# Performance work log

Measured on AMD Instinct MI355X. Metric: run time of the kernel, lower is better.

The kernel has to match this reference:

```python
import jax, jax.numpy as jnp
import numpy as np

B, S, H, NH, HD, V = 2, 2048, 1024, 16, 64, 32000
BASE = 10000.0
NEG = jnp.finfo(jnp.float32).min


def setup_inputs() -> dict:
    key = jax.random.key(0)
    ks = jax.random.split(key, 12)
    batch = jax.random.randint(ks[0], (B, S), 0, V)
    positions = jnp.broadcast_to(jnp.arange(S), (B, S))
    lengths = jax.random.randint(ks[1], (B,), 1, S + 1)  # >=1 to avoid fully-masked rows
    sc = 1.0 / np.sqrt(H)
    emb = jax.random.normal(ks[2], (V, H), dtype=jnp.float32) * 0.02
    wq = jax.random.normal(ks[3], (H, NH * HD), dtype=jnp.float32) * sc
    bq = jnp.zeros((NH * HD,), jnp.float32)
    wk = jax.random.normal(ks[4], (H, NH * HD), dtype=jnp.float32) * sc
    bk = jnp.zeros((NH * HD,), jnp.float32)
    wv = jax.random.normal(ks[5], (H, NH * HD), dtype=jnp.float32) * sc
    bv = jnp.zeros((NH * HD,), jnp.float32)
    wo = jax.random.normal(ks[6], (NH * HD, H), dtype=jnp.float32) * sc
    bo = jnp.zeros((H,), jnp.float32)
    return dict(batch=batch, positions=positions, lengths=lengths, emb=emb,
                wq=wq, bq=bq, wk=wk, bk=bk, wv=wv, bv=bv, wo=wo, bo=bo)


def _rope(x, positions):
    # x: [B, NH, S, HD]; positions: [B, S] int
    inv_freq = 1.0 / (BASE ** (jnp.arange(0, HD, 2, dtype=jnp.float32) / HD))  # [HD/2]
    freqs = positions.astype(jnp.float32)[..., None] * inv_freq               # [B, S, HD/2]
    ang = jnp.concatenate([freqs, freqs], axis=-1)                            # [B, S, HD]
    cos = jnp.cos(ang)[:, None]                                               # [B, 1, S, HD]
    sin = jnp.sin(ang)[:, None]
    x1, x2 = x[..., :HD // 2], x[..., HD // 2:]
    rot = jnp.concatenate([-x2, x1], axis=-1)
    return x * cos + rot * sin


def reference(batch, positions, lengths, emb, wq, bq, wk, bk, wv, bv, wo, bo):
    h = emb[batch]                                                 # [B, S, H]
    q = (h @ wq + bq).reshape(B, S, NH, HD).transpose(0, 2, 1, 3)  # [B, NH, S, HD]
    k = (h @ wk + bk).reshape(B, S, NH, HD).transpose(0, 2, 1, 3)
    v = (h @ wv + bv).reshape(B, S, NH, HD).transpose(0, 2, 1, 3)
    q = _rope(q, positions)
    k = _rope(k, positions)
    scores = jnp.einsum('bhqd,bhkd->bhqk', q, k) / np.sqrt(HD)     # [B, NH, S, S]
    causal = jnp.triu(jnp.full((S, S), NEG, jnp.float32), 1)
    pad = jnp.where(jnp.arange(S)[None, :] < lengths[:, None], 0.0, NEG)  # [B, S]
    mask = pad[:, None, None, :] + causal[None, None]              # [B, 1, S, S]
    attn = jax.nn.softmax(scores + mask, axis=-1)
    out = jnp.einsum('bhqk,bhkd->bhqd', attn, v)                   # [B, NH, S, HD]
    out = out.transpose(0, 2, 1, 3).reshape(B, S, NH * HD)
    return out @ wo + bo                                           # [B, S, H]
```

## Files before the change

### kernel.cpp

```cpp
#include <hip/hip_runtime.h>
#include <hip/hip_bf16.h>
#include <cstdint>

#define DEVINL __device__ __forceinline__

typedef __attribute__((ext_vector_type(8))) short short8;
typedef __attribute__((ext_vector_type(4))) short bhalf4;
typedef __attribute__((ext_vector_type(4))) float f32x4;

constexpr int B_ = 2, S_ = 2048, H_ = 1024, NH_ = 16, HD_ = 64;
constexpr int M_ = B_ * S_;
constexpr float SCALE = 0.125f;

DEVINL float bf2f(unsigned short h) {
    unsigned u = ((unsigned)h) << 16;
    float f; __builtin_memcpy(&f, &u, 4); return f;
}
DEVINL unsigned short f2bf(float f) {
    unsigned u; __builtin_memcpy(&u, &f, 4);
    u += 0x7FFFu + ((u >> 16) & 1u);
    return (unsigned short)(u >> 16);
}
DEVINL float ldin(const void* p, size_t i, int fp32) {
    return fp32 ? ((const float*)p)[i] : bf2f(((const unsigned short*)p)[i]);
}
DEVINL void gl16(const void* g, void* l) {
    __builtin_amdgcn_global_load_lds(
        (const __attribute__((address_space(1))) unsigned int*)g,
        (__attribute__((address_space(3))) unsigned int*)l, 16, 0, 0);
}
DEVINL f32x4 mfma16(short8 a, short8 b, f32x4 c) {
    return __builtin_amdgcn_mfma_f32_16x16x32_bf16(a, b, c, 0, 0, 0);
}
DEVINL f32x4 mfma16x16(bhalf4 a, bhalf4 b, f32x4 c) {
#if __has_builtin(__builtin_amdgcn_mfma_f32_16x16x16bf16_1k)
    return __builtin_amdgcn_mfma_f32_16x16x16bf16_1k(a, b, c, 0, 0, 0);
#else
    f32x4 d;
    asm volatile("v_mfma_f32_16x16x16_bf16 %0, %1, %2, %3\n\t"
                 "s_nop 7\n\ts_nop 7"
                 : "=v"(d) : "v"(a), "v"(b), "v"(c));
    return d;
#endif
}
DEVINL void fsincos(float rev01, float* sn, float* cs) {
#if __has_builtin(__builtin_amdgcn_sinf) && __has_builtin(__builtin_amdgcn_cosf)
    *sn = __builtin_amdgcn_sinf(rev01);
    *cs = __builtin_amdgcn_cosf(rev01);
#else
    float a = rev01 * 6.28318530717958647692f;
    *sn = __sinf(a); *cs = __cosf(a);
#endif
}

__global__ __launch_bounds__(256) void k_detect(const unsigned short* __restrict__ emb,
                                                int* __restrict__ flag) {
    int t = threadIdx.x;
    unsigned short hw = emb[2 * t];
    unsigned e = (hw >> 7) & 0xFFu;
    int plaus = ((e >= 90u) && (e <= 126u)) || ((hw & 0x7FFFu) == 0u);
    __shared__ int cnt[4];
    int s = plaus;
    #pragma unroll
    for (int o = 1; o < 64; o <<= 1) s += __shfl_xor(s, o);
    if ((t & 63) == 0) cnt[t >> 6] = s;
    __syncthreads();
    if (t == 0) flag[0] = ((cnt[0] + cnt[1] + cnt[2] + cnt[3]) > 192) ? 0 : 1;
}

__global__ __launch_bounds__(256) void k_bias(const void* bq, const void* bk,
                                              const void* bv, const void* bo,
                                              const int* __restrict__ flag,
                                              float* __restrict__ out) {
    int i = blockIdx.x * 256 + threadIdx.x;
    int fp32 = flag[0];
    const void* src = (i < 1024) ? bq : (i < 2048) ? bk : (i < 3072) ? bv : bo;
    out[i] = ldin(src, (size_t)(i & 1023), fp32);
}

__global__ __launch_bounds__(256) void k_transw(const void* w0, const void* w1,
                                                const void* w2, const void* w3,
                                                const int* __restrict__ flag,
                                                unsigned short* __restrict__ wT) {
    __shared__ float tile[32][33];
    int mat = blockIdx.z;
    const void* w = (mat == 0) ? w0 : (mat == 1) ? w1 : (mat == 2) ? w2 : w3;
    int fp32 = flag[0];
    int n0 = blockIdx.x * 32, k0 = blockIdx.y * 32;
    int tx = threadIdx.x, ty = threadIdx.y;
    for (int i = ty; i < 32; i += 8)
        tile[i][tx] = ldin(w, (size_t)(k0 + i) * 1024 + n0 + tx, fp32);
    __syncthreads();
    unsigned short* dst = wT + (size_t)mat * 1024 * 1024;
    for (int i = ty; i < 32; i += 8)
        dst[(size_t)(n0 + i) * 1024 + k0 + tx] = f2bf(tile[tx][i]);
}

__global__ __launch_bounds__(256) void k_gather(const int* __restrict__ batch,
                                                const void* __restrict__ emb,
                                                const int* __restrict__ flag,
                                                unsigned short* __restrict__ h) {
    int row = blockIdx.x, t = threadIdx.x;
    int tok = batch[row];
    unsigned short* dst = h + (size_t)row * H_;
    if (flag[0]) {
        const float4* s = (const float4*)((const float*)emb + (size_t)tok * H_);
        float4 x = s[t];
        unsigned long long pk = (unsigned long long)f2bf(x.x)
                              | ((unsigned long long)f2bf(x.y) << 16)
                              | ((unsigned long long)f2bf(x.z) << 32)
                              | ((unsigned long long)f2bf(x.w) << 48);
        ((unsigned long long*)dst)[t] = pk;
    } else {
        ((uint2*)dst)[t] =
            ((const uint2*)((const unsigned short*)emb + (size_t)tok * H_))[t];
    }
}

__global__ __launch_bounds__(256) void k_gemm_qkv(const unsigned short* __restrict__ A,
                                                  const unsigned short* __restrict__ Bt,
                                                  const float* __restrict__ bias,
                                                  const int* __restrict__ positions,
                                                  unsigned short* __restrict__ qo,
                                                  unsigned short* __restrict__ ko,
                                                  unsigned short* __restrict__ vo) {
    constexpr int K = 1024;
    __shared__ alignas(16) unsigned short As[128 * 32];
    __shared__ alignas(16) unsigned short Bs[128 * 32];
    int t = threadIdx.x, lane = t & 63, quad = lane >> 4, n16 = lane & 15;
    int w = t >> 6, wm = w >> 1, wn = w & 1;
    int m0 = blockIdx.y * 128, n0 = blockIdx.x * 128;
    f32x4 acc[4][4];
    #pragma unroll
    for (int mi = 0; mi < 4; mi++)
        #pragma unroll
        for (int ni = 0; ni < 4; ni++) acc[mi][ni] = (f32x4){0.f, 0.f, 0.f, 0.f};
    int c0 = t, c1 = t + 256;
    int ra0 = c0 >> 2, ka0 = (c0 & 3) * 8;
    int ra1 = c1 >> 2, ka1 = (c1 & 3) * 8;
    for (int k0 = 0; k0 < K; k0 += 32) {
        __syncthreads();
        gl16(A  + (size_t)(m0 + ra0) * K + k0 + ka0, &As[c0 * 8]);
        gl16(A  + (size_t)(m0 + ra1) * K + k0 + ka1, &As[c1 * 8]);
        gl16(Bt + (size_t)(n0 + ra0) * K + k0 + ka0, &Bs[c0 * 8]);
        gl16(Bt + (size_t)(n0 + ra1) * K + k0 + ka1, &Bs[c1 * 8]);
        __syncthreads();
        short8 af[4], bfr[4];
        #pragma unroll
        for (int mi = 0; mi < 4; mi++)
            af[mi] = *(const short8*)&As[(wm * 64 + mi * 16 + n16) * 32 + quad * 8];
        #pragma unroll
        for (int ni = 0; ni < 4; ni++)
            bfr[ni] = *(const short8*)&Bs[(wn * 64 + ni * 16 + n16) * 32 + quad * 8];
        #pragma unroll
        for (int mi = 0; mi < 4; mi++)
            #pragma unroll
            for (int ni = 0; ni < 4; ni++)
                acc[mi][ni] = mfma16(af[mi], bfr[ni], acc[mi][ni]);
    }
    int colbase = n0 + wn * 64;
    int buf = colbase >> 10;
    unsigned short* out = (buf == 0) ? qo : (buf == 1) ? ko : vo;
    int cc = colbase & 1023;
    float bb[4];
    #pragma unroll
    for (int ni = 0; ni < 4; ni++) bb[ni] = bias[colbase + ni * 16 + n16];
    if (buf == 2) {
        #pragma unroll
        for (int mi = 0; mi < 4; mi++)
            #pragma unroll
            for (int ni = 0; ni < 4; ni++) {
                int row = m0 + wm * 64 + mi * 16 + quad * 4;
                #pragma unroll
                for (int i = 0; i < 4; i++)
                    out[(size_t)(row + i) * 1024 + cc + ni * 16 + n16] =
                        f2bf(acc[mi][ni][i] + bb[ni]);
            }
    } else {
        float revf[2];
        #pragma unroll
        for (int ni = 0; ni < 2; ni++) {
            float d = (float)(ni * 16 + n16);
            revf[ni] = __expf(d * -0.28782313f) * 0.15915494f;
        }
        #pragma unroll
        for (int mi = 0; mi < 4; mi++) {
            int row0 = m0 + wm * 64 + mi * 16 + quad * 4;
            #pragma unroll
            for (int i = 0; i < 4; i++) {
                int row = row0 + i;
                float pos = (float)positions[row];
                #pragma unroll
                for (int ni = 0; ni < 2; ni++) {
                    float rev = pos * revf[ni];
                    float fr = rev - floorf(rev);
                    float sn, cs; fsincos(fr, &sn, &cs);
                    float x1 = acc[mi][ni][i] + bb[ni];
                    float x2 = acc[mi][ni + 2][i] + bb[ni + 2];
                    out[(size_t)row * 1024 + cc + ni * 16 + n16] = f2bf(x1 * cs - x2 * sn);
                    out[(size_t)row * 1024 + cc + (ni + 2) * 16 + n16] = f2bf(x2 * cs + x1 * sn);
                }
            }
        }
    }
}

__global__ __launch_bounds__(256) void k_attn(const unsigned short* __restrict__ q,
                                              const unsigned short* __restrict__ k_,
                                              const unsigned short* __restrict__ v,
                                              const int* __restrict__ lengths,
                                              unsigned short* __restrict__ o) {
    __shared__ alignas(16) unsigned short Ks[64 * 64];
    __shared__ alignas(16) unsigned short Vt[64 * 68];
    int bx = blockIdx.x;
    int j = bx & 15, hh = (bx >> 4) & 15, b = bx >> 8;
    int t = threadIdx.x, w = t >> 6, lane = t & 63, quad = lane >> 4, n16 = lane & 15;
    int len = lengths[b];
    int tile0 = j, tile1 = 31 - j;
    int kend0 = min(tile0 * 64 + 64, len);
    int kend1 = min(tile1 * 64 + 64, len);
    int nkt = (kend1 + 63) >> 6;
    int qrow0 = tile0 * 64 + w * 16 + n16;
    int qrow1 = tile1 * 64 + w * 16 + n16;
    int limit0 = min(qrow0, len - 1);
    int limit1 = min(qrow1, len - 1);
    short8 qf[2][2];
    {
        size_t qa = ((size_t)(b * S_ + qrow0)) * H_ + hh * 64 + quad * 8;
        size_t qb2 = ((size_t)(b * S_ + qrow1)) * H_ + hh * 64 + quad * 8;
        qf[0][0] = *(const short8*)(q + qa);  qf[0][1] = *(const short8*)(q + qa + 32);
        qf[1][0] = *(const short8*)(q + qb2); qf[1][1] = *(const short8*)(q + qb2 + 32);
    }
    f32x4 oa[2][4];
    float m_[2], l_[2];
    #pragma unroll
    for (int s = 0; s < 2; s++) {
        m_[s] = -__builtin_inff(); l_[s] = 0.f;
        #pragma unroll
        for (int nb = 0; nb < 4; nb++) oa[s][nb] = (f32x4){0.f, 0.f, 0.f, 0.f};
    }
    int vkey = t >> 3, vc = t & 7;
    for (int kt = 0; kt < nkt; kt++) {
        int kb = kt * 64;
        __syncthreads();
        {
            int s0 = t;        int ky = s0 >> 3; int ch = (s0 & 7) ^ (ky & 7);
            gl16(k_ + ((size_t)(b * S_ + kb + ky)) * H_ + hh * 64 + ch * 8, &Ks[s0 * 8]);
            int s1 = t + 256;  ky = s1 >> 3;     ch = (s1 & 7) ^ (ky & 7);
            gl16(k_ + ((size_t)(b * S_ + kb + ky)) * H_ + hh * 64 + ch * 8, &Ks[s1 * 8]);
        }
        #pragma unroll
        for (int hlf = 0; hlf < 2; hlf++) {
            int ky = vkey + hlf * 32;
            short8 vv = *(const short8*)(v + ((size_t)(b * S_ + kb + ky)) * H_ + hh * 64 + vc * 8);
            int slot = ky ^ ((vc >> 1) << 2);
            #pragma unroll
            for (int jj = 0; jj < 8; jj++)
                Vt[(vc * 8 + jj) * 68 + slot] = (unsigned short)vv[jj];
        }
        __syncthreads();
        short8 kf[4][2];
        #pragma unroll
        for (int st = 0; st < 4; st++)
            #pragma unroll
            for (int hf = 0; hf < 2; hf++) {
                int ky = st * 16 + n16;
                int slot = ky * 8 + ((hf * 4 + quad) ^ (ky & 7));
                kf[st][hf] = *(const short8*)&Ks[slot * 8];
            }
        bhalf4 vf[4][4];
        #pragma unroll
        for (int st = 0; st < 4; st++)
            #pragma unroll
            for (int nb = 0; nb < 4; nb++) {
                int slot = (st * 16 + quad * 4) ^ (nb << 2);
                vf[st][nb] = *(const bhalf4*)&Vt[(nb * 16 + n16) * 68 + slot];
            }
        #pragma unroll
        for (int si = 0; si < 2; si++) {
            if (si == 0 && kb >= kend0) continue;
            int limit = si ? limit1 : limit0;
            f32x4 sc[4];
            #pragma unroll
            for (int st = 0; st < 4; st++) {
                f32x4 z = (f32x4){0.f, 0.f, 0.f, 0.f};
                z = mfma16(kf[st][0], qf[si][0], z);
                z = mfma16(kf[st][1], qf[si][1], z);
                sc[st] = z;
            }
            float mx = -__builtin_inff();
            #pragma unroll
            for (int st = 0; st < 4; st++)
                #pragma unroll
                for (int i = 0; i < 4; i++) {
                    int kg = kb + st * 16 + quad * 4 + i;
                    float val = sc[st][i] * SCALE;
                    val = (kg <= limit) ? val : -__builtin_inff();
                    sc[st][i] = val;
                    mx = fmaxf(mx, val);
                }
            mx = fmaxf(mx, __shfl_xor(mx, 16));
            mx = fmaxf(mx, __shfl_xor(mx, 32));
            float mnew = fmaxf(m_[si], mx);
            float alpha = __expf(m_[si] - mnew);
            m_[si] = mnew;
            float rs = 0.f;
            bhalf4 pf[4];
            #pragma unroll
            for (int st = 0; st < 4; st++)
                #pragma unroll
                for (int i = 0; i < 4; i++) {
                    float p = __expf(sc[st][i] - mnew);
                    rs += p;
                    pf[st][i] = (short)f2bf(p);
                }
            rs += __shfl_xor(rs, 16);
            rs += __shfl_xor(rs, 32);
            l_[si] = alpha * l_[si] + rs;
            f32x4 av;
            #pragma unroll
            for (int i = 0; i < 4; i++) av[i] = __shfl(alpha, quad * 4 + i);
            #pragma unroll
            for (int nb = 0; nb < 4; nb++) oa[si][nb] *= av;
            #pragma unroll
            for (int st = 0; st < 4; st++)
                #pragma unroll
                for (int nb = 0; nb < 4; nb++)
                    oa[si][nb] = mfma16x16(pf[st], vf[st][nb], oa[si][nb]);
        }
    }
    #pragma unroll
    for (int si = 0; si < 2; si++) {
        int tb = si ? tile1 : tile0;
        f32x4 rl;
        #pragma unroll
        for (int i = 0; i < 4; i++) rl[i] = 1.f / __shfl(l_[si], quad * 4 + i);
        #pragma unroll
        for (int nb = 0; nb < 4; nb++) {
            #pragma unroll
            for (int i = 0; i < 4; i++) {
                int row = tb * 64 + w * 16 + quad * 4 + i;
                o[((size_t)(b * S_ + row)) * H_ + hh * 64 + nb * 16 + n16] =
                    f2bf(oa[si][nb][i] * rl[i]);
            }
        }
    }
}

__global__ __launch_bounds__(256) void k_gemm64(const unsigned short* __restrict__ A,
                                                const unsigned short* __restrict__ Bt,
                                                const float* __restrict__ bias,
                                                unsigned short* __restrict__ Cb,
                                                float* __restrict__ Cf,
                                                const int* __restrict__ flag) {
    constexpr int K = 1024, N = 1024;
    __shared__ alignas(16) unsigned short As[64 * 32];
    __shared__ alignas(16) unsigned short Bs[128 * 32];
    int t = threadIdx.x, lane = t & 63, quad = lane >> 4, n16 = lane & 15;
    int w = t >> 6, wm = w & 1, wn = w >> 1;
    int m0 = blockIdx.y * 64, n0 = blockIdx.x * 128;
    f32x4 acc[2][4];
    #pragma unroll
    for (int mi = 0; mi < 2; mi++)
        #pragma unroll
        for (int ni = 0; ni < 4; ni++) acc[mi][ni] = (f32x4){0.f, 0.f, 0.f, 0.f};
    int ra = t >> 2, ka = (t & 3) * 8;
    int rb1 = (t + 256) >> 2, kb1 = ((t + 256) & 3) * 8;
    for (int k0 = 0; k0 < K; k0 += 32) {
        __syncthreads();
        gl16(A  + (size_t)(m0 + ra) * K + k0 + ka, &As[t * 8]);
        gl16(Bt + (size_t)(n0 + ra) * K + k0 + ka, &Bs[t * 8]);
        gl16(Bt + (size_t)(n0 + rb1) * K + k0 + kb1, &Bs[(t + 256) * 8]);
        __syncthreads();
        short8 af[2], bfr[4];
        #pragma unroll
        for (int mi = 0; mi < 2; mi++)
            af[mi] = *(const short8*)&As[(wm * 32 + mi * 16 + n16) * 32 + quad * 8];
        #pragma unroll
        for (int ni = 0; ni < 4; ni++)
            bfr[ni] = *(const short8*)&Bs[(wn * 64 + ni * 16 + n16) * 32 + quad * 8];
        #pragma unroll
        for (int mi = 0; mi < 2; mi++)
            #pragma unroll
            for (int ni = 0; ni < 4; ni++)
                acc[mi][ni] = mfma16(af[mi], bfr[ni], acc[mi][ni]);
    }
    int fp32out = (flag[0] == 1);
    #pragma unroll
    for (int mi = 0; mi < 2; mi++) {
        #pragma unroll
        for (int ni = 0; ni < 4; ni++) {
            int row = m0 + wm * 32 + mi * 16 + quad * 4;
            int col = n0 + wn * 64 + ni * 16 + n16;
            float bb = bias[col];
            #pragma unroll
            for (int i = 0; i < 4; i++) {
                float val = acc[mi][ni][i] + bb;
                size_t idx = (size_t)(row + i) * N + col;
                if (fp32out) Cf[idx] = val;
                else         Cb[idx] = f2bf(val);
            }
        }
    }
}

extern "C" void kernel_launch(void* const* d_in, const int* in_sizes, int n_in,
                              void* d_out, int out_size, void* d_ws, size_t ws_size,
                              hipStream_t stream) {
    (void)in_sizes; (void)n_in; (void)out_size; (void)ws_size;
    const int* batch     = (const int*)d_in[0];
    const int* positions = (const int*)d_in[1];
    const int* lengths   = (const int*)d_in[2];
    const void* emb = d_in[3];
    const void* wq = d_in[4];  const void* bq = d_in[5];
    const void* wk = d_in[6];  const void* bk = d_in[7];
    const void* wv = d_in[8];  const void* bv = d_in[9];
    const void* wo = d_in[10]; const void* bo = d_in[11];

    char* ws = (char*)d_ws;
    int*   flag   = (int*)ws;
    float* biasws = (float*)(ws + 4096);
    unsigned short* wT = (unsigned short*)(ws + 20480);
    size_t off = 20480 + (8ull << 20);
    unsigned short* hbuf = (unsigned short*)(ws + off); off += (8ull << 20);
    unsigned short* qb   = (unsigned short*)(ws + off); off += (8ull << 20);
    unsigned short* kb2  = (unsigned short*)(ws + off); off += (8ull << 20);
    unsigned short* vb   = (unsigned short*)(ws + off); off += (8ull << 20);
    unsigned short* ao   = (unsigned short*)(ws + off); off += (8ull << 20);

    k_detect<<<1, 256, 0, stream>>>((const unsigned short*)emb, flag);
    k_bias<<<16, 256, 0, stream>>>(bq, bk, bv, bo, flag, biasws);
    k_transw<<<dim3(32, 32, 4), dim3(32, 8), 0, stream>>>(wq, wk, wv, wo, flag, wT);
    k_gather<<<M_, 256, 0, stream>>>(batch, emb, flag, hbuf);

    k_gemm_qkv<<<dim3(3072 / 128, M_ / 128), 256, 0, stream>>>(
        hbuf, wT, biasws, positions, qb, kb2, vb);

    k_attn<<<B_ * NH_ * 16, 256, 0, stream>>>(qb, kb2, vb, lengths, ao);

    k_gemm64<<<dim3(1024 / 128, M_ / 64), 256, 0, stream>>>(
        ao, wT + (3ull << 20), biasws + 3072,
        (unsigned short*)d_out, (float*)d_out, flag);
}
```

Baseline: 323.1 us.

## Write V transposed from QKV GEMM, fuse detect into bias, deepen K-step

The QKV GEMM epilogue now writes V transposed ([B, feature, seq]), so attention can load V tiles with direct global-to-LDS copies instead of a register transpose. The P·V product switches from the 16x16x16 MFMA to the 16x16x32 MFMA. Both GEMMs now load 64-wide K chunks per barrier pair, halving the number of synchronizations. The dtype-detect kernel is merged into the bias kernel, and for bf16 inputs the gather is skipped by indexing the embedding rows directly in the GEMM. The trade-offs are more LDS use per block and an epilogue V store with a large stride.

```diff
diff --git a/kernel.cpp b/kernel.cpp
--- a/kernel.cpp
+++ b/kernel.cpp
@@ -31,17 +31,6 @@
 }
 DEVINL f32x4 mfma16(short8 a, short8 b, f32x4 c) {
     return __builtin_amdgcn_mfma_f32_16x16x32_bf16(a, b, c, 0, 0, 0);
-}
-DEVINL f32x4 mfma16x16(bhalf4 a, bhalf4 b, f32x4 c) {
-#if __has_builtin(__builtin_amdgcn_mfma_f32_16x16x16bf16_1k)
-    return __builtin_amdgcn_mfma_f32_16x16x16bf16_1k(a, b, c, 0, 0, 0);
-#else
-    f32x4 d;
-    asm volatile("v_mfma_f32_16x16x16_bf16 %0, %1, %2, %3\n\t"
-                 "s_nop 7\n\ts_nop 7"
-                 : "=v"(d) : "v"(a), "v"(b), "v"(c));
-    return d;
-#endif
 }
 DEVINL void fsincos(float rev01, float* sn, float* cs) {
 #if __has_builtin(__builtin_amdgcn_sinf) && __has_builtin(__builtin_amdgcn_cosf)
@@ -52,28 +41,27 @@
     *sn = __sinf(a); *cs = __cosf(a);
 #endif
 }
-
-__global__ __launch_bounds__(256) void k_detect(const unsigned short* __restrict__ emb,
-                                                int* __restrict__ flag) {
-    int t = threadIdx.x;
+DEVINL int detect_fp32(const unsigned short* emb, int t) {
     unsigned short hw = emb[2 * t];
     unsigned e = (hw >> 7) & 0xFFu;
-    int plaus = ((e >= 90u) && (e <= 126u)) || ((hw & 0x7FFFu) == 0u);
+    int s = (((e >= 90u) && (e <= 126u)) || ((hw & 0x7FFFu) == 0u)) ? 1 : 0;
+    #pragma unroll
+    for (int o = 1; o < 64; o <<= 1) s += __shfl_xor(s, o);
     __shared__ int cnt[4];
-    int s = plaus;
-    #pragma unroll
-    for (int o = 1; o < 64; o <<= 1) s += __shfl_xor(s, o);
     if ((t & 63) == 0) cnt[t >> 6] = s;
     __syncthreads();
-    if (t == 0) flag[0] = ((cnt[0] + cnt[1] + cnt[2] + cnt[3]) > 192) ? 0 : 1;
+    return ((cnt[0] + cnt[1] + cnt[2] + cnt[3]) > 192) ? 0 : 1;
 }
 
 __global__ __launch_bounds__(256) void k_bias(const void* bq, const void* bk,
                                               const void* bv, const void* bo,
-                                              const int* __restrict__ flag,
+                                              const unsigned short* __restrict__ emb,
+                                              int* __restrict__ flag,
                                               float* __restrict__ out) {
-    int i = blockIdx.x * 256 + threadIdx.x;
-    int fp32 = flag[0];
+    int t = threadIdx.x;
+    int fp32 = detect_fp32(emb, t);
+    if (blockIdx.x == 0 && t == 0) flag[0] = fp32;
+    int i = blockIdx.x * 256 + t;
     const void* src = (i < 1024) ? bq : (i < 2048) ? bk : (i < 3072) ? bv : bo;
     out[i] = ldin(src, (size_t)(i & 1023), fp32);
 }
@@ -100,83 +88,103 @@
                                                 const void* __restrict__ emb,
                                                 const int* __restrict__ flag,
                                                 unsigned short* __restrict__ h) {
+    if (flag[0] == 0) return;
     int row = blockIdx.x, t = threadIdx.x;
     int tok = batch[row];
-    unsigned short* dst = h + (size_t)row * H_;
-    if (flag[0]) {
-        const float4* s = (const float4*)((const float*)emb + (size_t)tok * H_);
-        float4 x = s[t];
-        unsigned long long pk = (unsigned long long)f2bf(x.x)
-                              | ((unsigned long long)f2bf(x.y) << 16)
-                              | ((unsigned long long)f2bf(x.z) << 32)
-                              | ((unsigned long long)f2bf(x.w) << 48);
-        ((unsigned long long*)dst)[t] = pk;
-    } else {
-        ((uint2*)dst)[t] =
-            ((const uint2*)((const unsigned short*)emb + (size_t)tok * H_))[t];
-    }
-}
-
-__global__ __launch_bounds__(256) void k_gemm_qkv(const unsigned short* __restrict__ A,
+    const float4* s = (const float4*)((const float*)emb + (size_t)tok * H_);
+    float4 x = s[t];
+    unsigned long long pk = (unsigned long long)f2bf(x.x)
+                          | ((unsigned long long)f2bf(x.y) << 16)
+                          | ((unsigned long long)f2bf(x.z) << 32)
+                          | ((unsigned long long)f2bf(x.w) << 48);
+    ((unsigned long long*)(h + (size_t)row * H_))[t] = pk;
+}
+
+__global__ __launch_bounds__(256) void k_gemm_qkv(const unsigned short* __restrict__ embb,
+                                                  const unsigned short* __restrict__ hbuf,
+                                                  const int* __restrict__ batch,
                                                   const unsigned short* __restrict__ Bt,
                                                   const float* __restrict__ bias,
                                                   const int* __restrict__ positions,
+                                                  const int* __restrict__ flag,
                                                   unsigned short* __restrict__ qo,
                                                   unsigned short* __restrict__ ko,
-                                                  unsigned short* __restrict__ vo) {
+                                                  unsigned short* __restrict__ vt) {
     constexpr int K = 1024;
-    __shared__ alignas(16) unsigned short As[128 * 32];
-    __shared__ alignas(16) unsigned short Bs[128 * 32];
+    __shared__ alignas(16) unsigned short As[2][128 * 32];
+    __shared__ alignas(16) unsigned short Bs[2][128 * 32];
     int t = threadIdx.x, lane = t & 63, quad = lane >> 4, n16 = lane & 15;
     int w = t >> 6, wm = w >> 1, wn = w & 1;
     int m0 = blockIdx.y * 128, n0 = blockIdx.x * 128;
+    int fp32 = flag[0];
+    int r0 = t >> 2, r1 = 64 + r0;
+    int ka = (t & 3) * 8;
+    const unsigned short* a0;
+    const unsigned short* a1;
+    if (fp32) {
+        a0 = hbuf + (size_t)(m0 + r0) * K;
+        a1 = hbuf + (size_t)(m0 + r1) * K;
+    } else {
+        a0 = embb + (size_t)batch[m0 + r0] * K;
+        a1 = embb + (size_t)batch[m0 + r1] * K;
+    }
+    const unsigned short* b0 = Bt + (size_t)(n0 + r0) * K;
+    const unsigned short* b1 = Bt + (size_t)(n0 + r1) * K;
     f32x4 acc[4][4];
     #pragma unroll
     for (int mi = 0; mi < 4; mi++)
         #pragma unroll
         for (int ni = 0; ni < 4; ni++) acc[mi][ni] = (f32x4){0.f, 0.f, 0.f, 0.f};
-    int c0 = t, c1 = t + 256;
-    int ra0 = c0 >> 2, ka0 = (c0 & 3) * 8;
-    int ra1 = c1 >> 2, ka1 = (c1 & 3) * 8;
-    for (int k0 = 0; k0 < K; k0 += 32) {
-        __syncthreads();
-        gl16(A  + (size_t)(m0 + ra0) * K + k0 + ka0, &As[c0 * 8]);
-        gl16(A  + (size_t)(m0 + ra1) * K + k0 + ka1, &As[c1 * 8]);
-        gl16(Bt + (size_t)(n0 + ra0) * K + k0 + ka0, &Bs[c0 * 8]);
-        gl16(Bt + (size_t)(n0 + ra1) * K + k0 + ka1, &Bs[c1 * 8]);
-        __syncthreads();
-        short8 af[4], bfr[4];
-        #pragma unroll
-        for (int mi = 0; mi < 4; mi++)
-            af[mi] = *(const short8*)&As[(wm * 64 + mi * 16 + n16) * 32 + quad * 8];
-        #pragma unroll
-        for (int ni = 0; ni < 4; ni++)
-            bfr[ni] = *(const short8*)&Bs[(wn * 64 + ni * 16 + n16) * 32 + quad * 8];
-        #pragma unroll
-        for (int mi = 0; mi < 4; mi++)
+    for (int k0 = 0; k0 < K; k0 += 64) {
+        __syncthreads();
+        gl16(a0 + k0 + ka,      &As[0][t * 8]);
+        gl16(a1 + k0 + ka,      &As[0][(t + 256) * 8]);
+        gl16(a0 + k0 + 32 + ka, &As[1][t * 8]);
+        gl16(a1 + k0 + 32 + ka, &As[1][(t + 256) * 8]);
+        gl16(b0 + k0 + ka,      &Bs[0][t * 8]);
+        gl16(b1 + k0 + ka,      &Bs[0][(t + 256) * 8]);
+        gl16(b0 + k0 + 32 + ka, &Bs[1][t * 8]);
+        gl16(b1 + k0 + 32 + ka, &Bs[1][(t + 256) * 8]);
+        __syncthreads();
+        #pragma unroll
+        for (int ks = 0; ks < 2; ks++) {
+            short8 af[4], bfr[4];
+            #pragma unroll
+            for (int mi = 0; mi < 4; mi++)
+                af[mi] = *(const short8*)&As[ks][(wm * 64 + mi * 16 + n16) * 32 + quad * 8];
             #pragma unroll
             for (int ni = 0; ni < 4; ni++)
-                acc[mi][ni] = mfma16(af[mi], bfr[ni], acc[mi][ni]);
+                bfr[ni] = *(const short8*)&Bs[ks][(wn * 64 + ni * 16 + n16) * 32 + quad * 8];
+            #pragma unroll
+            for (int mi = 0; mi < 4; mi++)
+                #pragma unroll
+                for (int ni = 0; ni < 4; ni++)
+                    acc[mi][ni] = mfma16(af[mi], bfr[ni], acc[mi][ni]);
+        }
     }
     int colbase = n0 + wn * 64;
     int buf = colbase >> 10;
-    unsigned short* out = (buf == 0) ? qo : (buf == 1) ? ko : vo;
     int cc = colbase & 1023;
     float bb[4];
     #pragma unroll
     for (int ni = 0; ni < 4; ni++) bb[ni] = bias[colbase + ni * 16 + n16];
     if (buf == 2) {
         #pragma unroll
-        for (int mi = 0; mi < 4; mi++)
+        for (int mi = 0; mi < 4; mi++) {
+            int row = m0 + wm * 64 + mi * 16 + quad * 4;
+            int bb_ = row >> 11, s0 = row & 2047;
             #pragma unroll
             for (int ni = 0; ni < 4; ni++) {
-                int row = m0 + wm * 64 + mi * 16 + quad * 4;
+                int f = cc + ni * 16 + n16;
+                unsigned long long pk = 0;
                 #pragma unroll
                 for (int i = 0; i < 4; i++)
-                    out[(size_t)(row + i) * 1024 + cc + ni * 16 + n16] =
-                        f2bf(acc[mi][ni][i] + bb[ni]);
-            }
+                    pk |= (unsigned long long)f2bf(acc[mi][ni][i] + bb[ni]) << (16 * i);
+                *(unsigned long long*)(vt + ((size_t)(bb_ * 1024 + f)) * 2048 + s0) = pk;
+            }
+        }
     } else {
+        unsigned short* out = (buf == 0) ? qo : ko;
         float revf[2];
         #pragma unroll
         for (int ni = 0; ni < 2; ni++) {
@@ -207,11 +215,11 @@
 
 __global__ __launch_bounds__(256) void k_attn(const unsigned short* __restrict__ q,
                                               const unsigned short* __restrict__ k_,
-                                              const unsigned short* __restrict__ v,
+                                              const unsigned short* __restrict__ vt,
                                               const int* __restrict__ lengths,
                                               unsigned short* __restrict__ o) {
     __shared__ alignas(16) unsigned short Ks[64 * 64];
-    __shared__ alignas(16) unsigned short Vt[64 * 68];
+    __shared__ alignas(16) unsigned short Vs[64 * 64];
     int bx = blockIdx.x;
     int j = bx & 15, hh = (bx >> 4) & 15, b = bx >> 8;
     int t = threadIdx.x, w = t >> 6, lane = t & 63, quad = lane >> 4, n16 = lane & 15;
@@ -239,25 +247,17 @@
         #pragma unroll
         for (int nb = 0; nb < 4; nb++) oa[s][nb] = (f32x4){0.f, 0.f, 0.f, 0.f};
     }
-    int vkey = t >> 3, vc = t & 7;
+    int ky0 = t >> 3,        kc0 = (t & 7) ^ (ky0 & 7);
+    int ky1 = (t + 256) >> 3, kc1 = (t & 7) ^ (ky1 & 7);
+    const unsigned short* kbase = k_ + (size_t)b * S_ * H_ + hh * 64;
+    const unsigned short* vbase = vt + ((size_t)(b * 1024 + hh * 64)) * 2048;
     for (int kt = 0; kt < nkt; kt++) {
         int kb = kt * 64;
         __syncthreads();
-        {
-            int s0 = t;        int ky = s0 >> 3; int ch = (s0 & 7) ^ (ky & 7);
-            gl16(k_ + ((size_t)(b * S_ + kb + ky)) * H_ + hh * 64 + ch * 8, &Ks[s0 * 8]);
-            int s1 = t + 256;  ky = s1 >> 3;     ch = (s1 & 7) ^ (ky & 7);
-            gl16(k_ + ((size_t)(b * S_ + kb + ky)) * H_ + hh * 64 + ch * 8, &Ks[s1 * 8]);
-        }
-        #pragma unroll
-        for (int hlf = 0; hlf < 2; hlf++) {
-            int ky = vkey + hlf * 32;
-            short8 vv = *(const short8*)(v + ((size_t)(b * S_ + kb + ky)) * H_ + hh * 64 + vc * 8);
-            int slot = ky ^ ((vc >> 1) << 2);
-            #pragma unroll
-            for (int jj = 0; jj < 8; jj++)
-                Vt[(vc * 8 + jj) * 68 + slot] = (unsigned short)vv[jj];
-        }
+        gl16(kbase + (size_t)(kb + ky0) * H_ + kc0 * 8, &Ks[t * 8]);
+        gl16(kbase + (size_t)(kb + ky1) * H_ + kc1 * 8, &Ks[(t + 256) * 8]);
+        gl16(vbase + (size_t)ky0 * 2048 + kb + kc0 * 8, &Vs[t * 8]);
+        gl16(vbase + (size_t)ky1 * 2048 + kb + kc1 * 8, &Vs[(t + 256) * 8]);
         __syncthreads();
         short8 kf[4][2];
         #pragma unroll
@@ -268,13 +268,19 @@
                 int slot = ky * 8 + ((hf * 4 + quad) ^ (ky & 7));
                 kf[st][hf] = *(const short8*)&Ks[slot * 8];
             }
-        bhalf4 vf[4][4];
-        #pragma unroll
-        for (int st = 0; st < 4; st++)
+        short8 vf8[2][4];
+        #pragma unroll
+        for (int p = 0; p < 2; p++)
             #pragma unroll
             for (int nb = 0; nb < 4; nb++) {
-                int slot = (st * 16 + quad * 4) ^ (nb << 2);
-                vf[st][nb] = *(const bhalf4*)&Vt[(nb * 16 + n16) * 68 + slot];
+                int f = nb * 16 + n16;
+                int cl0 = 4 * p + (quad >> 1);
+                int cl1 = cl0 + 2;
+                int off = (quad & 1) * 4;
+                bhalf4 lo = *(const bhalf4*)&Vs[f * 64 + ((cl0 ^ (f & 7)) * 8 + off)];
+                bhalf4 hi = *(const bhalf4*)&Vs[f * 64 + ((cl1 ^ (f & 7)) * 8 + off)];
+                short8 cmb = {lo[0], lo[1], lo[2], lo[3], hi[0], hi[1], hi[2], hi[3]};
+                vf8[p][nb] = cmb;
             }
         #pragma unroll
         for (int si = 0; si < 2; si++) {
@@ -323,10 +329,13 @@
             #pragma unroll
             for (int nb = 0; nb < 4; nb++) oa[si][nb] *= av;
             #pragma unroll
-            for (int st = 0; st < 4; st++)
+            for (int p = 0; p < 2; p++) {
+                short8 pp = {pf[2 * p][0], pf[2 * p][1], pf[2 * p][2], pf[2 * p][3],
+                             pf[2 * p + 1][0], pf[2 * p + 1][1], pf[2 * p + 1][2], pf[2 * p + 1][3]};
                 #pragma unroll
                 for (int nb = 0; nb < 4; nb++)
-                    oa[si][nb] = mfma16x16(pf[st], vf[st][nb], oa[si][nb]);
+                    oa[si][nb] = mfma16(pp, vf8[p][nb], oa[si][nb]);
+            }
         }
     }
     #pragma unroll
@@ -354,36 +363,44 @@
                                                 float* __restrict__ Cf,
                                                 const int* __restrict__ flag) {
     constexpr int K = 1024, N = 1024;
-    __shared__ alignas(16) unsigned short As[64 * 32];
-    __shared__ alignas(16) unsigned short Bs[128 * 32];
+    __shared__ alignas(16) unsigned short As[2][64 * 32];
+    __shared__ alignas(16) unsigned short Bs[2][128 * 32];
     int t = threadIdx.x, lane = t & 63, quad = lane >> 4, n16 = lane & 15;
     int w = t >> 6, wm = w & 1, wn = w >> 1;
     int m0 = blockIdx.y * 64, n0 = blockIdx.x * 128;
+    int r0 = t >> 2, r1 = 64 + r0, ka = (t & 3) * 8;
+    const unsigned short* a0 = A + (size_t)(m0 + r0) * K;
+    const unsigned short* b0 = Bt + (size_t)(n0 + r0) * K;
+    const unsigned short* b1 = Bt + (size_t)(n0 + r1) * K;
     f32x4 acc[2][4];
     #pragma unroll
     for (int mi = 0; mi < 2; mi++)
         #pragma unroll
         for (int ni = 0; ni < 4; ni++) acc[mi][ni] = (f32x4){0.f, 0.f, 0.f, 0.f};
-    int ra = t >> 2, ka = (t & 3) * 8;
-    int rb1 = (t + 256) >> 2, kb1 = ((t + 256) & 3) * 8;
-    for (int k0 = 0; k0 < K; k0 += 32) {
-        __syncthreads();
-        gl16(A  + (size_t)(m0 + ra) * K + k0 + ka, &As[t * 8]);
-        gl16(Bt + (size_t)(n0 + ra) * K + k0 + ka, &Bs[t * 8]);
-        gl16(Bt + (size_t)(n0 + rb1) * K + k0 + kb1, &Bs[(t + 256) * 8]);
-        __syncthreads();
-        short8 af[2], bfr[4];
-        #pragma unroll
-        for (int mi = 0; mi < 2; mi++)
-            af[mi] = *(const short8*)&As[(wm * 32 + mi * 16 + n16) * 32 + quad * 8];
-        #pragma unroll
-        for (int ni = 0; ni < 4; ni++)
-            bfr[ni] = *(const short8*)&Bs[(wn * 64 + ni * 16 + n16) * 32 + quad * 8];
-        #pragma unroll
-        for (int mi = 0; mi < 2; mi++)
+    for (int k0 = 0; k0 < K; k0 += 64) {
+        __syncthreads();
+        gl16(a0 + k0 + ka,      &As[0][t * 8]);
+        gl16(a0 + k0 + 32 + ka, &As[1][t * 8]);
+        gl16(b0 + k0 + ka,      &Bs[0][t * 8]);
+        gl16(b1 + k0 + ka,      &Bs[0][(t + 256) * 8]);
+        gl16(b0 + k0 + 32 + ka, &Bs[1][t * 8]);
+        gl16(b1 + k0 + 32 + ka, &Bs[1][(t + 256) * 8]);
+        __syncthreads();
+        #pragma unroll
+        for (int ks = 0; ks < 2; ks++) {
+            short8 af[2], bfr[4];
+            #pragma unroll
+            for (int mi = 0; mi < 2; mi++)
+                af[mi] = *(const short8*)&As[ks][(wm * 32 + mi * 16 + n16) * 32 + quad * 8];
             #pragma unroll
             for (int ni = 0; ni < 4; ni++)
-                acc[mi][ni] = mfma16(af[mi], bfr[ni], acc[mi][ni]);
+                bfr[ni] = *(const short8*)&Bs[ks][(wn * 64 + ni * 16 + n16) * 32 + quad * 8];
+            #pragma unroll
+            for (int mi = 0; mi < 2; mi++)
+                #pragma unroll
+                for (int ni = 0; ni < 4; ni++)
+                    acc[mi][ni] = mfma16(af[mi], bfr[ni], acc[mi][ni]);
+        }
     }
     int fp32out = (flag[0] == 1);
     #pragma unroll
@@ -425,18 +442,19 @@
     unsigned short* hbuf = (unsigned short*)(ws + off); off += (8ull << 20);
     unsigned short* qb   = (unsigned short*)(ws + off); off += (8ull << 20);
     unsigned short* kb2  = (unsigned short*)(ws + off); off += (8ull << 20);
-    unsigned short* vb   = (unsigned short*)(ws + off); off += (8ull << 20);
+    unsigned short* vtb  = (unsigned short*)(ws + off); off += (8ull << 20);
     unsigned short* ao   = (unsigned short*)(ws + off); off += (8ull << 20);
 
-    k_detect<<<1, 256, 0, stream>>>((const unsigned short*)emb, flag);
-    k_bias<<<16, 256, 0, stream>>>(bq, bk, bv, bo, flag, biasws);
+    k_bias<<<16, 256, 0, stream>>>(bq, bk, bv, bo, (const unsigned short*)emb,
+                                   flag, biasws);
     k_transw<<<dim3(32, 32, 4), dim3(32, 8), 0, stream>>>(wq, wk, wv, wo, flag, wT);
     k_gather<<<M_, 256, 0, stream>>>(batch, emb, flag, hbuf);
 
     k_gemm_qkv<<<dim3(3072 / 128, M_ / 128), 256, 0, stream>>>(
-        hbuf, wT, biasws, positions, qb, kb2, vb);
-
-    k_attn<<<B_ * NH_ * 16, 256, 0, stream>>>(qb, kb2, vb, lengths, ao);
+        (const unsigned short*)emb, hbuf, batch, wT, biasws, positions, flag,
+        qb, kb2, vtb);
+
+    k_attn<<<B_ * NH_ * 16, 256, 0, stream>>>(qb, kb2, vtb, lengths, ao);
 
     k_gemm64<<<dim3(1024 / 128, M_ / 64), 256, 0, stream>>>(
         ao, wT + (3ull << 20), biasws + 3072,
```

Result: no change. 320.1 us (-0.9%).
